# Kernel optimization log

Hardware: AMD Instinct MI355X
Metric: run time of the kernel (lower is better)

Reference implementation:

```python
import jax, jax.numpy as jnp
import numpy as np

B, C, H, W = 32, 64, 64, 64
K = 512  # n_embeddings
D = 64   # embedding_dim


def setup_inputs() -> dict:
    key = jax.random.key(0)
    k1, k2 = jax.random.split(key)
    inputs = jax.random.normal(k1, (B, C, H, W), dtype=jnp.float32)
    embedding = jax.random.normal(k2, (K, D), dtype=jnp.float32)
    weight = jnp.ones((K,), dtype=jnp.float32)
    return {"inputs": inputs, "embedding": embedding, "weight": weight}


def reference(inputs, embedding, weight):
    # NCHW -> NHWC, flatten to [N, D]
    x = jnp.transpose(inputs, (0, 2, 3, 1))  # [B,H,W,D]
    input_shape = x.shape
    flat = x.reshape(-1, D)                  # [N,D], N = B*H*W
    n = flat.shape[0]

    usage = jnp.sum(weight >= 0.01)

    # squared Euclidean distances (argmin-equivalent to torch.cdist)
    d2 = (jnp.sum(flat * flat, axis=1, keepdims=True)
          - 2.0 * (flat @ embedding.T)
          + jnp.sum(embedding * embedding, axis=1))  # [N,K]
    indices = jnp.argmin(d2, axis=1)                 # [N]

    # one-hot assignment stats (scatter -> bincount form)
    counts = jnp.zeros((K,), dtype=flat.dtype).at[indices].add(1.0)
    avg_probs = counts / n
    perplexity = jnp.exp(-jnp.sum(avg_probs * jnp.log(avg_probs + 1e-10)))

    # straight-through quantization
    q = embedding[indices].reshape(input_shape)      # [B,H,W,D]
    quantized = jax.lax.stop_gradient(q) + x - jax.lax.stop_gradient(x)

    commitment_loss = jnp.mean((jax.lax.stop_gradient(quantized) - x) ** 2)

    quantized_nchw = jnp.transpose(quantized, (0, 3, 1, 2))
    return quantized_nchw, commitment_loss, perplexity, usage, indices
```

## Files before the change

### kernel.cpp

```cpp
#include <hip/hip_runtime.h>


typedef __attribute__((ext_vector_type(8))) _Float16 f16x8;
typedef __attribute__((ext_vector_type(4))) float f32x4;
typedef unsigned int uint;
typedef unsigned short ushort;

namespace {
constexpr int kC = 64, kH = 64, kW = 64;
constexpr int kK = 512, kD = 64;
constexpr int kHW = kH * kW;
constexpr int kCHW = kC * kHW;
constexpr int kN = 32 * kHW;
constexpr int kQElems = 32 * kC * kHW;
constexpr uint kGapFP = 21u;
}

__device__ __forceinline__ ushort hb(_Float16 h) { return __builtin_bit_cast(ushort, h); }
__device__ __forceinline__ uint umin(uint a, uint b) { return a < b ? a : b; }
__device__ __forceinline__ uint umax(uint a, uint b) { return a > b ? a : b; }

__device__ __forceinline__ void gld16(const void* g, void* l) {
  __builtin_amdgcn_global_load_lds(
      (const __attribute__((address_space(1))) uint*)g,
      (__attribute__((address_space(3))) uint*)l, 16, 0, 0);
}

__global__ __launch_bounds__(64) void vq_prep(const float* __restrict__ emb,
                                              ushort* __restrict__ embPh,
                                              ushort* __restrict__ embPl,
                                              float* __restrict__ embT,
                                              float* __restrict__ enorm,
                                              uint* __restrict__ counts,
                                              uint* __restrict__ flag_count) {
  const int k = blockIdx.x * 64 + threadIdx.x;
  const float4* __restrict__ ep4 = (const float4*)(emb + k * kD);
  float ev[kD];
  uint uh[32], ul[32];
  float s = 0.f;
#pragma unroll
  for (int j = 0; j < kD / 4; ++j) {
    const float4 v = ep4[j];
    ev[4 * j] = v.x; ev[4 * j + 1] = v.y; ev[4 * j + 2] = v.z; ev[4 * j + 3] = v.w;
    s = fmaf(v.x, v.x, s); s = fmaf(v.y, v.y, s);
    s = fmaf(v.z, v.z, s); s = fmaf(v.w, v.w, s);
#pragma unroll
    for (int t = 0; t < 2; ++t) {
      const float e0 = ev[4 * j + 2 * t] * 2048.f;
      const float e1 = ev[4 * j + 2 * t + 1] * 2048.f;
      const _Float16 h0 = (_Float16)e0, h1 = (_Float16)e1;
      const _Float16 l0 = (_Float16)(e0 - (float)h0);
      const _Float16 l1 = (_Float16)(e1 - (float)h1);
      uh[2 * j + t] = (uint)hb(h0) | ((uint)hb(h1) << 16);
      ul[2 * j + t] = (uint)hb(l0) | ((uint)hb(l1) << 16);
    }
  }
  uint4* __restrict__ ph4 = (uint4*)embPh;
  uint4* __restrict__ pl4 = (uint4*)embPl;
#pragma unroll
  for (int cc = 0; cc < 8; ++cc) {
    const int dst = k * 8 + (cc ^ (k & 7));
    ph4[dst] = uint4{uh[4 * cc], uh[4 * cc + 1], uh[4 * cc + 2], uh[4 * cc + 3]};
    pl4[dst] = uint4{ul[4 * cc], ul[4 * cc + 1], ul[4 * cc + 2], ul[4 * cc + 3]};
  }
#pragma unroll
  for (int c = 0; c < kD; ++c) embT[c * kK + k] = ev[c];
  enorm[k] = s;
  counts[k] = 0u;
  if (k == 0) *flag_count = 0u;
}

__global__ __launch_bounds__(512, 4) void vq_assign(
    const float* __restrict__ in, const ushort* __restrict__ embPh,
    const ushort* __restrict__ embPl, const float* __restrict__ embT,
    const float* __restrict__ enorm, float* __restrict__ idx_out,
    float* __restrict__ outq, uint* __restrict__ counts,
    float* __restrict__ partial, uint* __restrict__ flag_count,
    uint* __restrict__ flags, uint flag_cap) {
  __shared__ __align__(16) ushort xbh[128 * 64];
  __shared__ __align__(16) ushort xbl[128 * 64];
  __shared__ __align__(16) ushort ebh[2][4096];
  __shared__ __align__(16) ushort ebl[2][4096];
  __shared__ uint mm1[4][128], mm2[4][128];
  __shared__ float xnp[4][128];
  __shared__ uint hist[512];
  __shared__ uint fidx[128];

  const int tid = threadIdx.x;
  const int lane = tid & 63;
  const int wv = __builtin_amdgcn_readfirstlane(tid >> 6);
  const int ph = wv >> 2;
  const int cs = wv & 3;
  const int c = lane & 15;
  const int g = lane >> 4;

  const int blk = blockIdx.x;
  const int bb = blk >> 5;
  const int hw0 = (blk & 31) << 7;
  const float* __restrict__ xp = in + (size_t)bb * kCHW + hw0 + ph * 64;

  hist[tid] = 0u;

  auto stageE = [&](int buf, int st) {
    const size_t src = (size_t)st * 8192 + cs * 2048;
    const int dst = cs * 2048;
#pragma unroll
    for (int i = 0; i < 2; ++i) {
      gld16((const char*)embPh + src + i * 1024 + lane * 16,
            (char*)&ebh[buf][0] + dst + i * 1024);
      gld16((const char*)embPl + src + i * 1024 + lane * 16,
            (char*)&ebl[buf][0] + dst + i * 1024);
    }
  };
  stageE(0, 0);

  float en_pre[8];
#pragma unroll
  for (int st = 0; st < 8; ++st)
    en_pre[st] = (enorm[st * 64 + cs * 16 + c] + 256.f) * 2048.f;

  {
    const int p = lane;
    uint uh[8], ul[8];
    float xn = 0.f;
#pragma unroll
    for (int j = 0; j < 8; ++j) {
      const float f0 = xp[(size_t)(cs * 16 + 2 * j) * kHW + p];
      const float f1 = xp[(size_t)(cs * 16 + 2 * j + 1) * kHW + p];
      xn = fmaf(f0, f0, xn);
      xn = fmaf(f1, f1, xn);
      const float m0 = -2.f * f0, m1f = -2.f * f1;
      const _Float16 h0 = (_Float16)m0, h1 = (_Float16)m1f;
      const _Float16 l0 = (_Float16)(m0 - (float)h0);
      const _Float16 l1 = (_Float16)(m1f - (float)h1);
      uh[j] = (uint)hb(h0) | ((uint)hb(h1) << 16);
      ul[j] = (uint)hb(l0) | ((uint)hb(l1) << 16);
    }
    const int row = ph * 64 + p;
    const int swz = (row & 7) << 4;
    const int o0 = (row * 128 + cs * 32) ^ swz;
    const int o1 = (row * 128 + cs * 32 + 16) ^ swz;
    *(uint4*)((char*)xbh + o0) = uint4{uh[0], uh[1], uh[2], uh[3]};
    *(uint4*)((char*)xbh + o1) = uint4{uh[4], uh[5], uh[6], uh[7]};
    *(uint4*)((char*)xbl + o0) = uint4{ul[0], ul[1], ul[2], ul[3]};
    *(uint4*)((char*)xbl + o1) = uint4{ul[4], ul[5], ul[6], ul[7]};
    xnp[cs][row] = xn;
  }
  __syncthreads();

  uint m1[16], m2[16];
#pragma unroll
  for (int i = 0; i < 16; ++i) { m1[i] = 0xFFFFFFFFu; m2[i] = 0xFFFFFFFFu; }

#pragma unroll
  for (int st = 0; st < 8; ++st) {
    if (st < 7) stageE((st & 1) ^ 1, st + 1);

    if (st < 7) {
      asm volatile("s_waitcnt vmcnt(4)" ::: "memory");
    } else {
      asm volatile("s_waitcnt vmcnt(0)" ::: "memory");
    }
    __builtin_amdgcn_sched_barrier(0);

    const int rowb = cs * 16 + c;
    const int swb = (rowb & 7) << 4;
    const int ob0 = (rowb * 128 + g * 16) ^ swb;
    const int ob1 = (rowb * 128 + g * 16 + 64) ^ swb;
    const int bsel = st & 1;
    const f16x8 bh0 = *(const f16x8*)((const char*)&ebh[bsel][0] + ob0);
    const f16x8 bh1 = *(const f16x8*)((const char*)&ebh[bsel][0] + ob1);
    const f16x8 bl0 = *(const f16x8*)((const char*)&ebl[bsel][0] + ob0);
    const f16x8 bl1 = *(const f16x8*)((const char*)&ebl[bsel][0] + ob1);
    const float en = en_pre[st];
    const uint kor = (uint)(st * 64 + cs * 16 + c);
    __builtin_amdgcn_s_setprio(1);
#pragma unroll
    for (int rt = 0; rt < 4; ++rt) {
      f16x8 ah[2], al[2];
#pragma unroll
      for (int s = 0; s < 2; ++s) {
        const int row = ph * 64 + rt * 16 + c;
        const int off = (row * 128 + g * 16 + s * 64) ^ ((row & 7) << 4);
        ah[s] = *(const f16x8*)((const char*)xbh + off);
        al[s] = *(const f16x8*)((const char*)xbl + off);
      }
      f32x4 acc = {en, en, en, en};
      acc = __builtin_amdgcn_mfma_f32_16x16x32_f16(ah[0], bh0, acc, 0, 0, 0);
      acc = __builtin_amdgcn_mfma_f32_16x16x32_f16(ah[1], bh1, acc, 0, 0, 0);
      acc = __builtin_amdgcn_mfma_f32_16x16x32_f16(ah[0], bl0, acc, 0, 0, 0);
      acc = __builtin_amdgcn_mfma_f32_16x16x32_f16(ah[1], bl1, acc, 0, 0, 0);
      acc = __builtin_amdgcn_mfma_f32_16x16x32_f16(al[0], bh0, acc, 0, 0, 0);
      acc = __builtin_amdgcn_mfma_f32_16x16x32_f16(al[1], bh1, acc, 0, 0, 0);
#pragma unroll
      for (int r = 0; r < 4; ++r) {
        const uint u = ((uint)acc[r] << 9) | kor;
        const int i = rt * 4 + r;
        const uint t = umax(m1[i], u);
        m1[i] = umin(m1[i], u);
        m2[i] = umin(m2[i], t);
      }
    }
    __builtin_amdgcn_s_setprio(0);

    asm volatile("s_waitcnt lgkmcnt(0)" ::: "memory");
    __builtin_amdgcn_sched_barrier(0);
    __builtin_amdgcn_s_barrier();
  }

#pragma unroll
  for (int i = 0; i < 16; ++i) {
    uint a1 = m1[i], a2 = m2[i];
#pragma unroll
    for (int off = 1; off < 16; off <<= 1) {
      const uint o1 = __shfl_xor(a1, off, 64);
      const uint o2 = __shfl_xor(a2, off, 64);
      const uint t = umax(a1, o1);
      a1 = umin(a1, o1);
      a2 = umin(umin(a2, o2), t);
    }
    m1[i] = a1; m2[i] = a2;
  }

  if (c == 0) {
#pragma unroll
    for (int i = 0; i < 16; ++i) {
      const int p = ph * 64 + (i >> 2) * 16 + g * 4 + (i & 3);
      mm1[cs][p] = m1[i];
      mm2[cs][p] = m2[i];
    }
  }
  __syncthreads();

  if (tid < 128) {
    uint a1 = mm1[0][tid], a2 = mm2[0][tid];
#pragma unroll
    for (int s = 1; s < 4; ++s) {
      const uint u1 = mm1[s][tid], u2 = mm2[s][tid];
      const uint t = umax(a1, u1);
      a1 = umin(a1, u1);
      a2 = umin(umin(a2, u2), t);
    }
    const uint bidx = a1 & 511u;
    fidx[tid] = bidx;
    idx_out[blk * 128 + tid] = (float)bidx;
    if (((a2 >> 9) - (a1 >> 9)) < kGapFP) {
      const uint slot = atomicAdd(flag_count, 1u);
      if (slot < flag_cap) flags[slot] = (uint)(blk * 128 + tid);
    }
    atomicAdd(&hist[bidx], 1u);

    const float xnorm = (xnp[0][tid] + xnp[1][tid]) + (xnp[2][tid] + xnp[3][tid]);
    float d2 = fmaf((float)(a1 >> 9), 1.f / 2048.f, -256.f) + xnorm;
#pragma unroll
    for (int off = 32; off > 0; off >>= 1) d2 += __shfl_down(d2, off, 64);
    if ((tid & 63) == 0) partial[blk * 2 + (tid >> 6)] = d2;
  }
  __syncthreads();
  if (hist[tid]) atomicAdd(&counts[tid], hist[tid]);

  {
    const int ch = tid >> 3;
    const int wq = tid & 7;
    const float* __restrict__ tr = embT + ch * kK;
    float* __restrict__ oq = outq + (size_t)bb * kCHW + (size_t)ch * kHW + hw0 + wq * 16;
#pragma unroll
    for (int i = 0; i < 4; ++i) {
      const int p0 = wq * 16 + i * 4;
      float4 v;
      v.x = tr[fidx[p0 + 0]];
      v.y = tr[fidx[p0 + 1]];
      v.z = tr[fidx[p0 + 2]];
      v.w = tr[fidx[p0 + 3]];
      *(float4*)(oq + i * 4) = v;
    }
  }
}

__global__ __launch_bounds__(256) void vq_refine(const float* __restrict__ in,
                                                 const float* __restrict__ emb,
                                                 const uint* __restrict__ flag_count,
                                                 const uint* __restrict__ flags,
                                                 uint flag_cap,
                                                 float* __restrict__ idx_out,
                                                 float* __restrict__ outq) {
  uint cnt = *flag_count;
  if (cnt > flag_cap) cnt = flag_cap;
  const int lane = threadIdx.x & 63;
  const uint wave_id = blockIdx.x * 4u + (threadIdx.x >> 6);
  const uint wave_stride = gridDim.x * 4u;

  for (uint i = wave_id; i < cnt; i += wave_stride) {
    const int n = (int)flags[i];
    const int b = n >> 12;
    const int hw = n & 4095;
    const float* __restrict__ xp = in + (size_t)b * kCHW + hw;

    float xr[kD];
#pragma unroll
    for (int d = 0; d < kD; ++d) xr[d] = xp[(size_t)d * kHW];

    double best = 1e300;
    int bidx = 0;
#pragma unroll 1
    for (int kk = 0; kk < 8; ++kk) {
      const int k = lane * 8 + kk;
      const float4* __restrict__ ep4 = (const float4*)(emb + k * kD);
      double s0 = 0.0, s1 = 0.0;
#pragma unroll
      for (int j = 0; j < kD / 4; ++j) {
        const float4 e = ep4[j];
        const double d0 = (double)xr[4 * j + 0] - (double)e.x;
        const double d1 = (double)xr[4 * j + 1] - (double)e.y;
        const double d2 = (double)xr[4 * j + 2] - (double)e.z;
        const double d3 = (double)xr[4 * j + 3] - (double)e.w;
        s0 = fma(d0, d0, s0);
        s1 = fma(d1, d1, s1);
        s0 = fma(d2, d2, s0);
        s1 = fma(d3, d3, s1);
      }
      const double s = s0 + s1;
      if (s < best) { best = s; bidx = k; }
    }
#pragma unroll
    for (int off = 32; off > 0; off >>= 1) {
      const double ob = __shfl_xor(best, off, 64);
      const int oi = __shfl_xor(bidx, off, 64);
      if (ob < best || (ob == best && oi < bidx)) { best = ob; bidx = oi; }
    }
    if (lane == 0) idx_out[n] = (float)bidx;
    outq[(size_t)b * kCHW + (size_t)lane * kHW + hw] = emb[bidx * kD + lane];
  }
}

__global__ __launch_bounds__(512) void vq_finalize(const float* __restrict__ weight,
                                                   const uint* __restrict__ counts,
                                                   const float* __restrict__ partial,
                                                   float* __restrict__ out_scalars) {
  __shared__ float red[512];
  const int t = threadIdx.x;

  const float avg = (float)counts[t] / (float)kN;
  red[t] = avg * logf(avg + 1e-10f);
  __syncthreads();
#pragma unroll
  for (int off = 256; off > 0; off >>= 1) {
    if (t < off) red[t] += red[t + off];
    __syncthreads();
  }
  const float perp = expf(-red[0]);
  __syncthreads();

  red[t] = (partial[t] + partial[t + 512]) + (partial[t + 1024] + partial[t + 1536]);
  __syncthreads();
#pragma unroll
  for (int off = 256; off > 0; off >>= 1) {
    if (t < off) red[t] += red[t + off];
    __syncthreads();
  }
  const float loss = red[0] / (float)((long long)kN * (long long)kD);
  __syncthreads();

  red[t] = (weight[t] >= 0.01f) ? 1.f : 0.f;
  __syncthreads();
#pragma unroll
  for (int off = 256; off > 0; off >>= 1) {
    if (t < off) red[t] += red[t + off];
    __syncthreads();
  }
  if (t == 0) {
    out_scalars[0] = loss;
    out_scalars[1] = perp;
    out_scalars[2] = red[0];
  }
}

extern "C" void kernel_launch(void* const* d_in, const int* in_sizes, int n_in,
                              void* d_out, int out_size, void* d_ws, size_t ws_size,
                              hipStream_t stream) {
  const float* in = (const float*)d_in[0];
  const float* emb = (const float*)d_in[1];
  const float* weight = (const float*)d_in[2];
  float* out = (float*)d_out;

  float* ws_f = (float*)d_ws;
  uint* ws_u = (uint*)d_ws;
  ushort* embPh = (ushort*)d_ws;
  ushort* embPl = embPh + kK * kD;
  float* embT = ws_f + 32768;
  float* enorm = ws_f + 65536;
  uint* counts = ws_u + 66048;
  float* partial = ws_f + 66560;
  uint* flag_count = ws_u + 68608;
  uint* flags = ws_u + 68609;
  const size_t ws_elems = ws_size / 4;
  const uint flag_cap =
      (ws_elems > 68609)
          ? (uint)((ws_elems - 68609 < (size_t)kN) ? ws_elems - 68609 : (size_t)kN)
          : 0u;

  float* outq = out;
  float* out_scalars = out + kQElems;
  float* idx_out = out + kQElems + 3;

  vq_prep<<<8, 64, 0, stream>>>(emb, embPh, embPl, embT, enorm, counts, flag_count);
  vq_assign<<<kN / 128, 512, 0, stream>>>(in, embPh, embPl, embT, enorm, idx_out,
                                          outq, counts, partial, flag_count, flags,
                                          flag_cap);
  vq_refine<<<256, 256, 0, stream>>>(in, emb, flag_count, flags, flag_cap,
                                     idx_out, outq);
  vq_finalize<<<1, 512, 0, stream>>>(weight, counts, partial, out_scalars);
}
```

Before: 90.23 us.

## Repartition waves to 4x2 grid and alias LDS buffers to shrink footprint

The work split among the 8 waves changes from 2 row-halves by 4 codebook slices to 4 row-quarters by 2 codebook slices. Each wave now handles 32 rows against 16 codes per stage, over 16 stages of 32 codes, so each staged embedding tile is half as large. Post-loop scratch (mm1/mm2/fidx/hist) now aliases the embedding staging region in one flat LDS array, which cuts shared memory roughly in half and may allow more resident blocks per CU. The costs are twice as many pipeline stages and barriers, and the final cross-slice min reduction shrinks from 4 slices to 2.

```diff
diff --git a/kernel.cpp b/kernel.cpp
--- a/kernel.cpp
+++ b/kernel.cpp
@@ -77,47 +77,46 @@
     float* __restrict__ outq, uint* __restrict__ counts,
     float* __restrict__ partial, uint* __restrict__ flag_count,
     uint* __restrict__ flags, uint flag_cap) {
-  __shared__ __align__(16) ushort xbh[128 * 64];
-  __shared__ __align__(16) ushort xbl[128 * 64];
-  __shared__ __align__(16) ushort ebh[2][4096];
-  __shared__ __align__(16) ushort ebl[2][4096];
-  __shared__ uint mm1[4][128], mm2[4][128];
-  __shared__ float xnp[4][128];
-  __shared__ uint hist[512];
-  __shared__ uint fidx[128];
+  __shared__ __align__(16) char lds[51200];
+  char* __restrict__ xbh = lds;
+  char* __restrict__ xbl = lds + 16384;
+  char* __restrict__ ebh = lds + 32768;
+  char* __restrict__ ebl = lds + 40960;
+  float* __restrict__ xnp = (float*)(lds + 49152);
+  uint* __restrict__ mm1 = (uint*)(lds + 32768);
+  uint* __restrict__ mm2 = (uint*)(lds + 33792);
+  uint* __restrict__ fidx = (uint*)(lds + 34816);
+  uint* __restrict__ hist = (uint*)(lds + 35328);
 
   const int tid = threadIdx.x;
   const int lane = tid & 63;
   const int wv = __builtin_amdgcn_readfirstlane(tid >> 6);
-  const int ph = wv >> 2;
-  const int cs = wv & 3;
+  const int sph = wv >> 2;
+  const int scs = wv & 3;
+  const int cph = wv >> 1;
+  const int ccs = wv & 1;
   const int c = lane & 15;
   const int g = lane >> 4;
 
   const int blk = blockIdx.x;
   const int bb = blk >> 5;
   const int hw0 = (blk & 31) << 7;
-  const float* __restrict__ xp = in + (size_t)bb * kCHW + hw0 + ph * 64;
-
-  hist[tid] = 0u;
+  const float* __restrict__ xp = in + (size_t)bb * kCHW + hw0 + sph * 64;
 
   auto stageE = [&](int buf, int st) {
-    const size_t src = (size_t)st * 8192 + cs * 2048;
-    const int dst = cs * 2048;
-#pragma unroll
-    for (int i = 0; i < 2; ++i) {
-      gld16((const char*)embPh + src + i * 1024 + lane * 16,
-            (char*)&ebh[buf][0] + dst + i * 1024);
-      gld16((const char*)embPl + src + i * 1024 + lane * 16,
-            (char*)&ebl[buf][0] + dst + i * 1024);
-    }
+    const size_t src = (size_t)st * 4096 + ccs * 2048;
+    const int dst = buf * 4096 + ccs * 2048;
+    gld16((const char*)embPh + src + lane * 16, ebh + dst);
+    gld16((const char*)embPh + src + 1024 + lane * 16, ebh + dst + 1024);
+    gld16((const char*)embPl + src + lane * 16, ebl + dst);
+    gld16((const char*)embPl + src + 1024 + lane * 16, ebl + dst + 1024);
   };
   stageE(0, 0);
 
-  float en_pre[8];
-#pragma unroll
-  for (int st = 0; st < 8; ++st)
-    en_pre[st] = (enorm[st * 64 + cs * 16 + c] + 256.f) * 2048.f;
+  float en_pre[16];
+#pragma unroll
+  for (int st = 0; st < 16; ++st)
+    en_pre[st] = (enorm[st * 32 + ccs * 16 + c] + 256.f) * 2048.f;
 
   {
     const int p = lane;
@@ -125,8 +124,8 @@
     float xn = 0.f;
 #pragma unroll
     for (int j = 0; j < 8; ++j) {
-      const float f0 = xp[(size_t)(cs * 16 + 2 * j) * kHW + p];
-      const float f1 = xp[(size_t)(cs * 16 + 2 * j + 1) * kHW + p];
+      const float f0 = xp[(size_t)(scs * 16 + 2 * j) * kHW + p];
+      const float f1 = xp[(size_t)(scs * 16 + 2 * j + 1) * kHW + p];
       xn = fmaf(f0, f0, xn);
       xn = fmaf(f1, f1, xn);
       const float m0 = -2.f * f0, m1f = -2.f * f1;
@@ -136,54 +135,54 @@
       uh[j] = (uint)hb(h0) | ((uint)hb(h1) << 16);
       ul[j] = (uint)hb(l0) | ((uint)hb(l1) << 16);
     }
-    const int row = ph * 64 + p;
+    const int row = sph * 64 + p;
     const int swz = (row & 7) << 4;
-    const int o0 = (row * 128 + cs * 32) ^ swz;
-    const int o1 = (row * 128 + cs * 32 + 16) ^ swz;
-    *(uint4*)((char*)xbh + o0) = uint4{uh[0], uh[1], uh[2], uh[3]};
-    *(uint4*)((char*)xbh + o1) = uint4{uh[4], uh[5], uh[6], uh[7]};
-    *(uint4*)((char*)xbl + o0) = uint4{ul[0], ul[1], ul[2], ul[3]};
-    *(uint4*)((char*)xbl + o1) = uint4{ul[4], ul[5], ul[6], ul[7]};
-    xnp[cs][row] = xn;
-  }
-  __syncthreads();
-
-  uint m1[16], m2[16];
-#pragma unroll
-  for (int i = 0; i < 16; ++i) { m1[i] = 0xFFFFFFFFu; m2[i] = 0xFFFFFFFFu; }
-
-#pragma unroll
-  for (int st = 0; st < 8; ++st) {
-    if (st < 7) stageE((st & 1) ^ 1, st + 1);
-
-    if (st < 7) {
+    const int o0 = (row * 128 + scs * 32) ^ swz;
+    const int o1 = (row * 128 + scs * 32 + 16) ^ swz;
+    *(uint4*)(xbh + o0) = uint4{uh[0], uh[1], uh[2], uh[3]};
+    *(uint4*)(xbh + o1) = uint4{uh[4], uh[5], uh[6], uh[7]};
+    *(uint4*)(xbl + o0) = uint4{ul[0], ul[1], ul[2], ul[3]};
+    *(uint4*)(xbl + o1) = uint4{ul[4], ul[5], ul[6], ul[7]};
+    xnp[scs * 128 + row] = xn;
+  }
+  __syncthreads();
+
+  uint m1[8], m2[8];
+#pragma unroll
+  for (int i = 0; i < 8; ++i) { m1[i] = 0xFFFFFFFFu; m2[i] = 0xFFFFFFFFu; }
+
+#pragma unroll
+  for (int st = 0; st < 16; ++st) {
+    if (st < 15) stageE((st & 1) ^ 1, st + 1);
+
+    if (st < 15) {
       asm volatile("s_waitcnt vmcnt(4)" ::: "memory");
     } else {
       asm volatile("s_waitcnt vmcnt(0)" ::: "memory");
     }
     __builtin_amdgcn_sched_barrier(0);
 
-    const int rowb = cs * 16 + c;
+    const int rowb = ccs * 16 + c;
     const int swb = (rowb & 7) << 4;
-    const int ob0 = (rowb * 128 + g * 16) ^ swb;
-    const int ob1 = (rowb * 128 + g * 16 + 64) ^ swb;
-    const int bsel = st & 1;
-    const f16x8 bh0 = *(const f16x8*)((const char*)&ebh[bsel][0] + ob0);
-    const f16x8 bh1 = *(const f16x8*)((const char*)&ebh[bsel][0] + ob1);
-    const f16x8 bl0 = *(const f16x8*)((const char*)&ebl[bsel][0] + ob0);
-    const f16x8 bl1 = *(const f16x8*)((const char*)&ebl[bsel][0] + ob1);
+    const int bbase = (st & 1) * 4096;
+    const int ob0 = bbase + ((rowb * 128 + g * 16) ^ swb);
+    const int ob1 = bbase + ((rowb * 128 + g * 16 + 64) ^ swb);
+    const f16x8 bh0 = *(const f16x8*)(ebh + ob0);
+    const f16x8 bh1 = *(const f16x8*)(ebh + ob1);
+    const f16x8 bl0 = *(const f16x8*)(ebl + ob0);
+    const f16x8 bl1 = *(const f16x8*)(ebl + ob1);
     const float en = en_pre[st];
-    const uint kor = (uint)(st * 64 + cs * 16 + c);
+    const uint kor = (uint)(st * 32 + ccs * 16 + c);
     __builtin_amdgcn_s_setprio(1);
 #pragma unroll
-    for (int rt = 0; rt < 4; ++rt) {
+    for (int rt = 0; rt < 2; ++rt) {
       f16x8 ah[2], al[2];
 #pragma unroll
       for (int s = 0; s < 2; ++s) {
-        const int row = ph * 64 + rt * 16 + c;
+        const int row = cph * 32 + rt * 16 + c;
         const int off = (row * 128 + g * 16 + s * 64) ^ ((row & 7) << 4);
-        ah[s] = *(const f16x8*)((const char*)xbh + off);
-        al[s] = *(const f16x8*)((const char*)xbl + off);
+        ah[s] = *(const f16x8*)(xbh + off);
+        al[s] = *(const f16x8*)(xbl + off);
       }
       f32x4 acc = {en, en, en, en};
       acc = __builtin_amdgcn_mfma_f32_16x16x32_f16(ah[0], bh0, acc, 0, 0, 0);
@@ -209,7 +208,7 @@
   }
 
 #pragma unroll
-  for (int i = 0; i < 16; ++i) {
+  for (int i = 0; i < 8; ++i) {
     uint a1 = m1[i], a2 = m2[i];
 #pragma unroll
     for (int off = 1; off < 16; off <<= 1) {
@@ -224,19 +223,20 @@
 
   if (c == 0) {
 #pragma unroll
-    for (int i = 0; i < 16; ++i) {
-      const int p = ph * 64 + (i >> 2) * 16 + g * 4 + (i & 3);
-      mm1[cs][p] = m1[i];
-      mm2[cs][p] = m2[i];
-    }
-  }
+    for (int i = 0; i < 8; ++i) {
+      const int rt = i >> 2, r = i & 3;
+      const int p = cph * 32 + rt * 16 + g * 4 + r;
+      mm1[ccs * 128 + p] = m1[i];
+      mm2[ccs * 128 + p] = m2[i];
+    }
+  }
+  hist[tid] = 0u;
   __syncthreads();
 
   if (tid < 128) {
-    uint a1 = mm1[0][tid], a2 = mm2[0][tid];
-#pragma unroll
-    for (int s = 1; s < 4; ++s) {
-      const uint u1 = mm1[s][tid], u2 = mm2[s][tid];
+    uint a1 = mm1[tid], a2 = mm2[tid];
+    {
+      const uint u1 = mm1[128 + tid], u2 = mm2[128 + tid];
       const uint t = umax(a1, u1);
       a1 = umin(a1, u1);
       a2 = umin(umin(a2, u2), t);
@@ -250,7 +250,7 @@
     }
     atomicAdd(&hist[bidx], 1u);
 
-    const float xnorm = (xnp[0][tid] + xnp[1][tid]) + (xnp[2][tid] + xnp[3][tid]);
+    const float xnorm = (xnp[tid] + xnp[128 + tid]) + (xnp[256 + tid] + xnp[384 + tid]);
     float d2 = fmaf((float)(a1 >> 9), 1.f / 2048.f, -256.f) + xnorm;
 #pragma unroll
     for (int off = 32; off > 0; off >>= 1) d2 += __shfl_down(d2, off, 64);
```

Result: no change. 91.12 us (+1.0%).
